# Performance work log

Measured on AMD Instinct MI355X. Metric: run time of the kernel, lower is better.

## Reference

```python
import jax, jax.numpy as jnp
import numpy as np

EMB, HID, NH = 512, 256, 8
DH = HID // NH
LN_EPS = 1e-5


def _mk(key, shape, scale=0.02):
    return jax.random.normal(key, shape, dtype=jnp.float32) * scale


def setup_inputs() -> dict:
    key = jax.random.key(0)
    ks = jax.random.split(key, 24)
    B, S = 8, 256
    return {
        "memory_embeddings": jax.random.normal(ks[0], (B, S, EMB), dtype=jnp.float32),
        # memory_encoder: Linear(512,256) -> LayerNorm -> ReLU -> Linear(256,256)
        "enc_w1": _mk(ks[1], (HID, EMB)), "enc_b1": jnp.zeros((HID,), jnp.float32),
        "ln_g": jnp.ones((HID,), jnp.float32), "ln_b": jnp.zeros((HID,), jnp.float32),
        "enc_w2": _mk(ks[2], (HID, HID)), "enc_b2": jnp.zeros((HID,), jnp.float32),
        # MultiheadAttention packed qkv + out proj
        "in_proj_w": _mk(ks[3], (3 * HID, HID)), "in_proj_b": jnp.zeros((3 * HID,), jnp.float32),
        "out_w": _mk(ks[4], (HID, HID)), "out_b": jnp.zeros((HID,), jnp.float32),
        # consistency head: Linear(256,128) -> ReLU -> Linear(128,1) -> Sigmoid
        "cons_w1": _mk(ks[5], (HID // 2, HID)), "cons_b1": jnp.zeros((HID // 2,), jnp.float32),
        "cons_w2": _mk(ks[6], (1, HID // 2)), "cons_b2": jnp.zeros((1,), jnp.float32),
        # hallucination detector
        "hall_w1": _mk(ks[7], (HID // 2, HID)), "hall_b1": jnp.zeros((HID // 2,), jnp.float32),
        "hall_w2": _mk(ks[8], (1, HID // 2)), "hall_b2": jnp.zeros((1,), jnp.float32),
        # contradiction analyzer: Linear(512,256) -> ReLU -> Linear(256,1) -> Sigmoid
        "con_w1": _mk(ks[9], (HID, 2 * HID)), "con_b1": jnp.zeros((HID,), jnp.float32),
        "con_w2": _mk(ks[10], (1, HID)), "con_b2": jnp.zeros((1,), jnp.float32),
    }


def _forward(memory_embeddings, enc_w1, enc_b1, ln_g, ln_b, enc_w2, enc_b2,
             in_proj_w, in_proj_b, out_w, out_b,
             cons_w1, cons_b1, cons_w2, cons_b2,
             hall_w1, hall_b1, hall_w2, hall_b2,
             con_w1, con_b1, con_w2, con_b2):
    B, S, _ = memory_embeddings.shape
    # --- memory encoder (dropout in eval mode = identity) ---
    h = memory_embeddings @ enc_w1.T + enc_b1                      # [B,S,HID]
    mu = h.mean(-1, keepdims=True)
    var = ((h - mu) ** 2).mean(-1, keepdims=True)
    h = (h - mu) * jax.lax.rsqrt(var + LN_EPS) * ln_g + ln_b
    mf = jax.nn.relu(h) @ enc_w2.T + enc_b2                        # [B,S,HID]
    # --- multihead self-attention (batch_first, averaged attn weights) ---
    qkv = mf @ in_proj_w.T + in_proj_b                              # [B,S,3H]
    q, k, v = jnp.split(qkv, 3, axis=-1)
    def heads(t):  # [B,S,H] -> [B,NH,S,DH]
        return t.reshape(B, S, NH, DH).transpose(0, 2, 1, 3)
    q, k, v = heads(q), heads(k), heads(v)
    scores = jnp.einsum('bhsd,bhtd->bhst', q, k) / jnp.sqrt(jnp.float32(DH))
    attn = jax.nn.softmax(scores, axis=-1)                          # [B,NH,S,S]
    ctx = jnp.einsum('bhst,bhtd->bhsd', attn, v)
    ctx = ctx.transpose(0, 2, 1, 3).reshape(B, S, HID)
    attended = ctx @ out_w.T + out_b                                # [B,S,HID]
    attn_weights = attn.mean(axis=1)                                # [B,S,S]
    # --- pooled heads ---
    pooled = attended.mean(axis=1)                                  # [B,HID]
    cons = jax.nn.sigmoid(jax.nn.relu(pooled @ cons_w1.T + cons_b1) @ cons_w2.T + cons_b2)[:, 0]
    hall = jax.nn.sigmoid(jax.nn.relu(pooled @ hall_w1.T + hall_b1) @ hall_w2.T + hall_b2)[:, 0]
    # --- contradiction matrix over all i<j pairs (vectorized gather/MLP/scatter) ---
    iu, ju = np.triu_indices(S, k=1)                                # static indices
    Wa, Wb = con_w1[:, :HID], con_w1[:, HID:]                       # split concat-linear
    a = mf @ Wa.T                                                   # [B,S,HID]
    b = mf @ Wb.T
    hid = jax.nn.relu(a[:, iu] + b[:, ju] + con_b1)                 # [B,P,HID]
    sc = jax.nn.sigmoid(hid @ con_w2.T + con_b2)[..., 0]            # [B,P]
    M = jnp.zeros((B, S, S), dtype=mf.dtype)
    M = M.at[:, iu, ju].set(sc)
    M = M.at[:, ju, iu].set(sc)
    return cons, hall, M, attn_weights


def reference(memory_embeddings, enc_w1, enc_b1, ln_g, ln_b, enc_w2, enc_b2,
              in_proj_w, in_proj_b, out_w, out_b,
              cons_w1, cons_b1, cons_w2, cons_b2,
              hall_w1, hall_b1, hall_w2, hall_b2,
              con_w1, con_b1, con_w2, con_b2):
    return _forward(memory_embeddings, enc_w1, enc_b1, ln_g, ln_b, enc_w2, enc_b2,
                    in_proj_w, in_proj_b, out_w, out_b,
                    cons_w1, cons_b1, cons_w2, cons_b2,
                    hall_w1, hall_b1, hall_w2, hall_b2,
                    con_w1, con_b1, con_w2, con_b2)
```

## Files before the change

### kernel.cpp

```cpp
#include <hip/hip_runtime.h>
#include <math.h>

typedef __attribute__((ext_vector_type(8))) short bf16x8;
typedef __attribute__((ext_vector_type(4))) float f32x4;

__device__ __forceinline__ short f2b(float f) {
  union { float f; unsigned u; } v; v.f = f;
  unsigned u = v.u + 0x7fffu + ((v.u >> 16) & 1u);
  return (short)(u >> 16);
}

__device__ __forceinline__ bf16x8 cvt8(float4 a, float4 b) {
  bf16x8 r;
  r[0] = f2b(a.x); r[1] = f2b(a.y); r[2] = f2b(a.z); r[3] = f2b(a.w);
  r[4] = f2b(b.x); r[5] = f2b(b.y); r[6] = f2b(b.z); r[7] = f2b(b.w);
  return r;
}

__global__ __launch_bounds__(512) void k_enc(
    const float* __restrict__ me,
    const float* __restrict__ w1f, const float* __restrict__ b1,
    const float* __restrict__ g, const float* __restrict__ lb,
    const float* __restrict__ w2f, const float* __restrict__ b2,
    unsigned short* __restrict__ mfb, float* __restrict__ poolctx) {
  __shared__ float hh[16 * 260];
  __shared__ unsigned short rA[16 * 264];
  __shared__ unsigned short mfs[16 * 256];
  int tid = threadIdx.x, lane = tid & 63, w = tid >> 6;
  int row0 = blockIdx.x * 16;
  int m = lane & 15, q = lane >> 4;
  if (blockIdx.x == 0) {
    float4 z = {0.f, 0.f, 0.f, 0.f};
    ((float4*)poolctx)[tid] = z;
  }
  {
    f32x4 acc0 = (f32x4){0.f, 0.f, 0.f, 0.f};
    f32x4 acc1 = (f32x4){0.f, 0.f, 0.f, 0.f};
    const float* ap = me + (size_t)(row0 + m) * 512 + q * 8;
    const float* bp0 = w1f + (size_t)(w * 32 + m) * 512 + q * 8;
    const float* bp1 = w1f + (size_t)(w * 32 + 16 + m) * 512 + q * 8;
    float4 pa[4][2], pb[4][2][2];
#pragma unroll
    for (int d = 0; d < 4; ++d) {
      pa[d][0] = *(const float4*)(ap + d * 32);
      pa[d][1] = *(const float4*)(ap + d * 32 + 4);
      pb[d][0][0] = *(const float4*)(bp0 + d * 32);
      pb[d][0][1] = *(const float4*)(bp0 + d * 32 + 4);
      pb[d][1][0] = *(const float4*)(bp1 + d * 32);
      pb[d][1][1] = *(const float4*)(bp1 + d * 32 + 4);
    }
#pragma unroll
    for (int it = 0; it < 16; ++it) {
      int slot = it & 3;
      float4 a0 = pa[slot][0], a1 = pa[slot][1];
      float4 b00 = pb[slot][0][0], b01 = pb[slot][0][1];
      float4 b10 = pb[slot][1][0], b11 = pb[slot][1][1];
      if (it + 4 < 16) {
        pa[slot][0] = *(const float4*)(ap + (it + 4) * 32);
        pa[slot][1] = *(const float4*)(ap + (it + 4) * 32 + 4);
        pb[slot][0][0] = *(const float4*)(bp0 + (it + 4) * 32);
        pb[slot][0][1] = *(const float4*)(bp0 + (it + 4) * 32 + 4);
        pb[slot][1][0] = *(const float4*)(bp1 + (it + 4) * 32);
        pb[slot][1][1] = *(const float4*)(bp1 + (it + 4) * 32 + 4);
      }
      bf16x8 af = cvt8(a0, a1);
      acc0 = __builtin_amdgcn_mfma_f32_16x16x32_bf16(af, cvt8(b00, b01), acc0, 0, 0, 0);
      acc1 = __builtin_amdgcn_mfma_f32_16x16x32_bf16(af, cvt8(b10, b11), acc1, 0, 0, 0);
    }
#pragma unroll
    for (int nt = 0; nt < 2; ++nt) {
      int col = w * 32 + nt * 16 + m;
      float bias = b1[col];
      f32x4 a = nt ? acc1 : acc0;
#pragma unroll
      for (int reg = 0; reg < 4; ++reg)
        hh[(q * 4 + reg) * 260 + col] = a[reg] + bias;
    }
  }
  __syncthreads();
  {
    float4 g4 = *(const float4*)(g + lane * 4);
    float4 lb4 = *(const float4*)(lb + lane * 4);
#pragma unroll
    for (int rr = 0; rr < 2; ++rr) {
      int r = w * 2 + rr;
      float4 v = *(const float4*)&hh[r * 260 + lane * 4];
      float s1 = v.x + v.y + v.z + v.w;
      float s2 = v.x * v.x + v.y * v.y + v.z * v.z + v.w * v.w;
#pragma unroll
      for (int o = 32; o > 0; o >>= 1) {
        s1 += __shfl_xor(s1, o, 64);
        s2 += __shfl_xor(s2, o, 64);
      }
      float mu = s1 * (1.f / 256.f);
      float var = s2 * (1.f / 256.f) - mu * mu;
      float rs = rsqrtf(var + 1e-5f);
      unsigned short y0 = (unsigned short)f2b(fmaxf((v.x - mu) * rs * g4.x + lb4.x, 0.f));
      unsigned short y1 = (unsigned short)f2b(fmaxf((v.y - mu) * rs * g4.y + lb4.y, 0.f));
      unsigned short y2 = (unsigned short)f2b(fmaxf((v.z - mu) * rs * g4.z + lb4.z, 0.f));
      unsigned short y3 = (unsigned short)f2b(fmaxf((v.w - mu) * rs * g4.w + lb4.w, 0.f));
      uint2 pk;
      pk.x = (unsigned)y0 | ((unsigned)y1 << 16);
      pk.y = (unsigned)y2 | ((unsigned)y3 << 16);
      *(uint2*)&rA[r * 264 + lane * 4] = pk;
    }
  }
  __syncthreads();
  {
    f32x4 acc0 = (f32x4){0.f, 0.f, 0.f, 0.f};
    f32x4 acc1 = (f32x4){0.f, 0.f, 0.f, 0.f};
    const float* cp0 = w2f + (size_t)(w * 32 + m) * 256 + q * 8;
    const float* cp1 = w2f + (size_t)(w * 32 + 16 + m) * 256 + q * 8;
    float4 pb[4][2][2];
#pragma unroll
    for (int d = 0; d < 4; ++d) {
      pb[d][0][0] = *(const float4*)(cp0 + d * 32);
      pb[d][0][1] = *(const float4*)(cp0 + d * 32 + 4);
      pb[d][1][0] = *(const float4*)(cp1 + d * 32);
      pb[d][1][1] = *(const float4*)(cp1 + d * 32 + 4);
    }
#pragma unroll
    for (int it = 0; it < 8; ++it) {
      int slot = it & 3;
      float4 b00 = pb[slot][0][0], b01 = pb[slot][0][1];
      float4 b10 = pb[slot][1][0], b11 = pb[slot][1][1];
      if (it + 4 < 8) {
        pb[slot][0][0] = *(const float4*)(cp0 + (it + 4) * 32);
        pb[slot][0][1] = *(const float4*)(cp0 + (it + 4) * 32 + 4);
        pb[slot][1][0] = *(const float4*)(cp1 + (it + 4) * 32);
        pb[slot][1][1] = *(const float4*)(cp1 + (it + 4) * 32 + 4);
      }
      bf16x8 af = *(const bf16x8*)&rA[m * 264 + it * 32 + q * 8];
      acc0 = __builtin_amdgcn_mfma_f32_16x16x32_bf16(af, cvt8(b00, b01), acc0, 0, 0, 0);
      acc1 = __builtin_amdgcn_mfma_f32_16x16x32_bf16(af, cvt8(b10, b11), acc1, 0, 0, 0);
    }
#pragma unroll
    for (int nt = 0; nt < 2; ++nt) {
      int col = w * 32 + nt * 16 + m;
      float bias = b2[col];
      f32x4 a = nt ? acc1 : acc0;
#pragma unroll
      for (int reg = 0; reg < 4; ++reg)
        mfs[(q * 4 + reg) * 256 + col] = (unsigned short)f2b(a[reg] + bias);
    }
  }
  __syncthreads();
  {
    const uint4* src = (const uint4*)mfs;
    uint4* dst = (uint4*)(mfb + (size_t)row0 * 256);
    dst[tid] = src[tid];
  }
}

__global__ __launch_bounds__(256) void k_proj5(
    const unsigned short* __restrict__ mfb,
    const float* __restrict__ wq, const float* __restrict__ wc,
    const float* __restrict__ bq, const float* __restrict__ cb1,
    float* __restrict__ qkv, float* __restrict__ amat,
    float* __restrict__ bmat) {
  int tid = threadIdx.x, lane = tid & 63, w = tid >> 6;
  int row0 = blockIdx.x * 16;
  int part = blockIdx.y;
  int m = lane & 15, q = lane >> 4;
  const float* Wbase;
  size_t wstride;
  if (part < 3) { Wbase = wq + (size_t)part * 256 * 256; wstride = 256; }
  else { Wbase = wc + (part == 4 ? 256 : 0); wstride = 512; }
  bf16x8 a[8];
#pragma unroll
  for (int ks = 0; ks < 8; ++ks)
    a[ks] = *(const bf16x8*)(mfb + (size_t)(row0 + m) * 256 + ks * 32 + q * 8);
  f32x4 acc[4];
#pragma unroll
  for (int i = 0; i < 4; ++i) acc[i] = (f32x4){0.f, 0.f, 0.f, 0.f};
  const float* bp[4];
#pragma unroll
  for (int nt = 0; nt < 4; ++nt)
    bp[nt] = Wbase + (size_t)(w * 64 + nt * 16 + m) * wstride + q * 8;
  float4 pb[4][4][2];
#pragma unroll
  for (int d = 0; d < 4; ++d)
#pragma unroll
    for (int nt = 0; nt < 4; ++nt) {
      pb[d][nt][0] = *(const float4*)(bp[nt] + d * 32);
      pb[d][nt][1] = *(const float4*)(bp[nt] + d * 32 + 4);
    }
#pragma unroll
  for (int it = 0; it < 8; ++it) {
    int slot = it & 3;
    float4 b0l = pb[slot][0][0], b0h = pb[slot][0][1];
    float4 b1l = pb[slot][1][0], b1h = pb[slot][1][1];
    float4 b2l = pb[slot][2][0], b2h = pb[slot][2][1];
    float4 b3l = pb[slot][3][0], b3h = pb[slot][3][1];
    if (it + 4 < 8) {
#pragma unroll
      for (int nt = 0; nt < 4; ++nt) {
        pb[slot][nt][0] = *(const float4*)(bp[nt] + (it + 4) * 32);
        pb[slot][nt][1] = *(const float4*)(bp[nt] + (it + 4) * 32 + 4);
      }
    }
    acc[0] = __builtin_amdgcn_mfma_f32_16x16x32_bf16(a[it], cvt8(b0l, b0h), acc[0], 0, 0, 0);
    acc[1] = __builtin_amdgcn_mfma_f32_16x16x32_bf16(a[it], cvt8(b1l, b1h), acc[1], 0, 0, 0);
    acc[2] = __builtin_amdgcn_mfma_f32_16x16x32_bf16(a[it], cvt8(b2l, b2h), acc[2], 0, 0, 0);
    acc[3] = __builtin_amdgcn_mfma_f32_16x16x32_bf16(a[it], cvt8(b3l, b3h), acc[3], 0, 0, 0);
  }
#pragma unroll
  for (int nt = 0; nt < 4; ++nt) {
    int col = w * 64 + nt * 16 + m;
    float bias;
    float* dst;
    int ld;
    if (part < 3) { bias = bq[part * 256 + col]; dst = qkv + part * 256; ld = 768; }
    else if (part == 3) { bias = cb1[col]; dst = amat; ld = 256; }
    else { bias = 0.f; dst = bmat; ld = 256; }
#pragma unroll
    for (int reg = 0; reg < 4; ++reg) {
      int row = row0 + q * 4 + reg;
      dst[(size_t)row * ld + col] = acc[nt][reg] + bias;
    }
  }
}

__global__ __launch_bounds__(256) void k_attn_mfma(
    const float* __restrict__ qkv, unsigned short* __restrict__ attnb,
    float* __restrict__ poolctx) {
  __shared__ unsigned short qs[32 * 40];
  __shared__ unsigned short kb[256 * 40];
  __shared__ unsigned short vt[32 * 264];
  __shared__ unsigned short ps[32 * 264];
  __shared__ float redm[2][32];
  __shared__ float reds[2][32];
  int blk = blockIdx.x;
  int sg = blk & 7, bh = blk >> 3, h = bh & 7, b = bh >> 3;
  int tid = threadIdx.x, lane = tid & 63, w = tid >> 6;
  int m = lane & 15, q = lane >> 4;
  {
    int r = tid >> 3, c4 = tid & 7;
    float4 v = *(const float4*)(qkv + ((size_t)(b * 256 + sg * 32 + r)) * 768 + h * 32 + c4 * 4);
    unsigned short* dst = &qs[r * 40 + c4 * 4];
    dst[0] = (unsigned short)f2b(v.x); dst[1] = (unsigned short)f2b(v.y);
    dst[2] = (unsigned short)f2b(v.z); dst[3] = (unsigned short)f2b(v.w);
  }
#pragma unroll
  for (int i = 0; i < 8; ++i) {
    int f = i * 256 + tid;
    int r = f >> 3, c4 = f & 7;
    float4 v = *(const float4*)(qkv + ((size_t)(b * 256 + r)) * 768 + 256 + h * 32 + c4 * 4);
    unsigned short* dst = &kb[r * 40 + c4 * 4];
    dst[0] = (unsigned short)f2b(v.x); dst[1] = (unsigned short)f2b(v.y);
    dst[2] = (unsigned short)f2b(v.z); dst[3] = (unsigned short)f2b(v.w);
  }
  {
    const float4* vr = (const float4*)(qkv + ((size_t)(b * 256 + tid)) * 768 + 512 + h * 32);
#pragma unroll
    for (int d4 = 0; d4 < 8; ++d4) {
      float4 vv = vr[d4];
      vt[(d4 * 4 + 0) * 264 + tid] = (unsigned short)f2b(vv.x);
      vt[(d4 * 4 + 1) * 264 + tid] = (unsigned short)f2b(vv.y);
      vt[(d4 * 4 + 2) * 264 + tid] = (unsigned short)f2b(vv.z);
      vt[(d4 * 4 + 3) * 264 + tid] = (unsigned short)f2b(vv.w);
    }
  }
  __syncthreads();
  int mt = w & 1, ng = w >> 1;
  int lrow = mt * 16 + q * 4;
  f32x4 acc[8];
  {
    bf16x8 af = *(const bf16x8*)&qs[(mt * 16 + m) * 40 + q * 8];
#pragma unroll
    for (int nt = 0; nt < 8; ++nt) {
      bf16x8 bf = *(const bf16x8*)&kb[(ng * 128 + nt * 16 + m) * 40 + q * 8];
      acc[nt] = __builtin_amdgcn_mfma_f32_16x16x32_bf16(
          af, bf, (f32x4){0.f, 0.f, 0.f, 0.f}, 0, 0, 0);
    }
  }
  const float scale = 0.17677669529663689f;
#pragma unroll
  for (int nt = 0; nt < 8; ++nt)
#pragma unroll
    for (int reg = 0; reg < 4; ++reg) acc[nt][reg] *= scale;
  float pm[4];
#pragma unroll
  for (int reg = 0; reg < 4; ++reg) {
    float mx = acc[0][reg];
#pragma unroll
    for (int nt = 1; nt < 8; ++nt) mx = fmaxf(mx, acc[nt][reg]);
#pragma unroll
    for (int o = 1; o < 16; o <<= 1) mx = fmaxf(mx, __shfl_xor(mx, o, 64));
    pm[reg] = mx;
  }
  if (m == 0) {
#pragma unroll
    for (int reg = 0; reg < 4; ++reg) redm[ng][lrow + reg] = pm[reg];
  }
  __syncthreads();
  float inv[4];
  float psum[4];
#pragma unroll
  for (int reg = 0; reg < 4; ++reg) {
    float Mv = fmaxf(redm[0][lrow + reg], redm[1][lrow + reg]);
    float s = 0.f;
#pragma unroll
    for (int nt = 0; nt < 8; ++nt) {
      float e = __expf(acc[nt][reg] - Mv);
      acc[nt][reg] = e;
      s += e;
    }
#pragma unroll
    for (int o = 1; o < 16; o <<= 1) s += __shfl_xor(s, o, 64);
    psum[reg] = s;
  }
  if (m == 0) {
#pragma unroll
    for (int reg = 0; reg < 4; ++reg) reds[ng][lrow + reg] = psum[reg];
  }
  __syncthreads();
#pragma unroll
  for (int reg = 0; reg < 4; ++reg)
    inv[reg] = 1.f / (reds[0][lrow + reg] + reds[1][lrow + reg]);
#pragma unroll
  for (int nt = 0; nt < 8; ++nt) {
    int t = ng * 128 + nt * 16 + m;
#pragma unroll
    for (int reg = 0; reg < 4; ++reg)
      ps[(lrow + reg) * 264 + t] = (unsigned short)f2b(acc[nt][reg] * inv[reg]);
  }
  __syncthreads();
  {
    int r = tid >> 3, seg = tid & 7;
    const uint4* src = (const uint4*)&ps[r * 264 + seg * 32];
    uint4* dst = (uint4*)(attnb + ((size_t)(bh * 256 + sg * 32 + r)) * 256 + seg * 32);
    dst[0] = src[0]; dst[1] = src[1]; dst[2] = src[2]; dst[3] = src[3];
  }
  {
    int dt = w >> 1;
    f32x4 a = (f32x4){0.f, 0.f, 0.f, 0.f};
#pragma unroll
    for (int ks = 0; ks < 256; ks += 32) {
      bf16x8 af = *(const bf16x8*)&ps[(mt * 16 + m) * 264 + ks + q * 8];
      bf16x8 bf = *(const bf16x8*)&vt[(dt * 16 + m) * 264 + ks + q * 8];
      a = __builtin_amdgcn_mfma_f32_16x16x32_bf16(af, bf, a, 0, 0, 0);
    }
    float colsum = a[0] + a[1] + a[2] + a[3];
    colsum += __shfl_xor(colsum, 16, 64);
    colsum += __shfl_xor(colsum, 32, 64);
    if (lane < 16)
      atomicAdd(&poolctx[b * 256 + h * 32 + dt * 16 + m], colsum);
  }
}

__global__ __launch_bounds__(256) void k_tail(
    const float* __restrict__ amat, const float* __restrict__ bmat,
    const float* __restrict__ conw2, const float* __restrict__ conb2,
    float* __restrict__ M,
    const unsigned short* __restrict__ attnb, float* __restrict__ out_aw,
    const float* __restrict__ poolctx,
    const float* __restrict__ outw, const float* __restrict__ outb,
    const float* __restrict__ cw1, const float* __restrict__ cb1h,
    const float* __restrict__ cw2, const float* __restrict__ cb2,
    const float* __restrict__ hw1, const float* __restrict__ hb1,
    const float* __restrict__ hw2, const float* __restrict__ hb2,
    float* __restrict__ out) {
  __shared__ float smem[32 * 132 * 2 + 256];
  int bx = blockIdx.x, tid = threadIdx.x;
  if (bx < 288) {
    float* As = smem;
    float* Bs = smem + 32 * 132;
    float* w2s = smem + 32 * 132 * 2;
    int b = bx / 36, tix = bx % 36;
    int it = 0, rem = tix;
    while (rem >= 8 - it) { rem -= 8 - it; ++it; }
    int jt = it + rem;
    int tj = tid & 15, ti = tid >> 4;
    w2s[tid] = conw2[tid];
    float acc00 = 0, acc01 = 0, acc10 = 0, acc11 = 0;
    const float* Ab = amat + ((size_t)(b * 256 + it * 32)) * 256;
    const float* Bb = bmat + ((size_t)(b * 256 + jt * 32)) * 256;
    for (int ch = 0; ch < 2; ++ch) {
      __syncthreads();
#pragma unroll
      for (int k = 0; k < 4; ++k) {
        int f = tid + k * 256;
        int r = f >> 5, c4 = f & 31;
        float4 va = *(const float4*)(Ab + (size_t)r * 256 + ch * 128 + c4 * 4);
        float4 vb = *(const float4*)(Bb + (size_t)r * 256 + ch * 128 + c4 * 4);
        *(float4*)&As[r * 132 + c4 * 4] = va;
        *(float4*)&Bs[r * 132 + c4 * 4] = vb;
      }
      __syncthreads();
      const float* a0 = As + (2 * ti) * 132;
      const float* a1 = a0 + 132;
      const float* b0 = Bs + (2 * tj) * 132;
      const float* b1 = b0 + 132;
      const float* w2c = w2s + ch * 128;
      for (int d = 0; d < 128; d += 4) {
        float4 wv = *(const float4*)&w2c[d];
        float4 av0 = *(const float4*)&a0[d];
        float4 av1 = *(const float4*)&a1[d];
        float4 bv0 = *(const float4*)&b0[d];
        float4 bv1 = *(const float4*)&b1[d];
        acc00 += fmaxf(av0.x + bv0.x, 0.f) * wv.x + fmaxf(av0.y + bv0.y, 0.f) * wv.y
               + fmaxf(av0.z + bv0.z, 0.f) * wv.z + fmaxf(av0.w + bv0.w, 0.f) * wv.w;
        acc01 += fmaxf(av0.x + bv1.x, 0.f) * wv.x + fmaxf(av0.y + bv1.y, 0.f) * wv.y
               + fmaxf(av0.z + bv1.z, 0.f) * wv.z + fmaxf(av0.w + bv1.w, 0.f) * wv.w;
        acc10 += fmaxf(av1.x + bv0.x, 0.f) * wv.x + fmaxf(av1.y + bv0.y, 0.f) * wv.y
               + fmaxf(av1.z + bv0.z, 0.f) * wv.z + fmaxf(av1.w + bv0.w, 0.f) * wv.w;
        acc11 += fmaxf(av1.x + bv1.x, 0.f) * wv.x + fmaxf(av1.y + bv1.y, 0.f) * wv.y
               + fmaxf(av1.z + bv1.z, 0.f) * wv.z + fmaxf(av1.w + bv1.w, 0.f) * wv.w;
      }
    }
    float c2 = conb2[0];
    float s00 = 1.f / (1.f + expf(-(acc00 + c2)));
    float s01 = 1.f / (1.f + expf(-(acc01 + c2)));
    float s10 = 1.f / (1.f + expf(-(acc10 + c2)));
    float s11 = 1.f / (1.f + expf(-(acc11 + c2)));
    float* Mb = M + ((size_t)b << 16);
    int i0 = it * 32 + 2 * ti, i1 = i0 + 1;
    int j0 = jt * 32 + 2 * tj, j1 = j0 + 1;
    if (it != jt) {
      Mb[i0 * 256 + j0] = s00; Mb[j0 * 256 + i0] = s00;
      Mb[i0 * 256 + j1] = s01; Mb[j1 * 256 + i0] = s01;
      Mb[i1 * 256 + j0] = s10; Mb[j0 * 256 + i1] = s10;
      Mb[i1 * 256 + j1] = s11; Mb[j1 * 256 + i1] = s11;
    } else {
      if (j0 > i0) { Mb[i0 * 256 + j0] = s00; Mb[j0 * 256 + i0] = s00; }
      else if (j0 == i0) Mb[i0 * 256 + j0] = 0.f;
      if (j1 > i0) { Mb[i0 * 256 + j1] = s01; Mb[j1 * 256 + i0] = s01; }
      if (j0 > i1) { Mb[i1 * 256 + j0] = s10; Mb[j0 * 256 + i1] = s10; }
      if (j1 > i1) { Mb[i1 * 256 + j1] = s11; Mb[j1 * 256 + i1] = s11; }
      else if (j1 == i1) Mb[i1 * 256 + j1] = 0.f;
    }
  } else if (bx < 544) {
    int gid = (bx - 288) * 256 + tid;
    int b = gid >> 13, e8 = gid & 8191;
    size_t e = (size_t)e8 * 8;
    float s0 = 0, s1 = 0, s2 = 0, s3 = 0, s4 = 0, s5 = 0, s6 = 0, s7 = 0;
#pragma unroll
    for (int h = 0; h < 8; ++h) {
      uint4 v = *(const uint4*)(attnb + (((size_t)(b * 8 + h)) << 16) + e);
      s0 += __uint_as_float(v.x << 16); s1 += __uint_as_float(v.x & 0xffff0000u);
      s2 += __uint_as_float(v.y << 16); s3 += __uint_as_float(v.y & 0xffff0000u);
      s4 += __uint_as_float(v.z << 16); s5 += __uint_as_float(v.z & 0xffff0000u);
      s6 += __uint_as_float(v.w << 16); s7 += __uint_as_float(v.w & 0xffff0000u);
    }
    float* dst = out_aw + ((size_t)b << 16) + e;
    float4 r0 = {s0 * 0.125f, s1 * 0.125f, s2 * 0.125f, s3 * 0.125f};
    float4 r1 = {s4 * 0.125f, s5 * 0.125f, s6 * 0.125f, s7 * 0.125f};
    *(float4*)dst = r0;
    *(float4*)(dst + 4) = r1;
  } else {
    float* pc = smem;
    float* psh = smem + 256;
    float* red = smem + 512;
    int b = bx - 544, j = tid;
    pc[j] = poolctx[b * 256 + j] * (1.f / 256.f);
    __syncthreads();
    float s = outb[j];
    const float4* wr = (const float4*)(outw + (size_t)j * 256);
    for (int k4 = 0; k4 < 64; ++k4) {
      float4 wv = wr[k4];
      const float* p = pc + k4 * 4;
      s += p[0] * wv.x + p[1] * wv.y + p[2] * wv.z + p[3] * wv.w;
    }
    psh[j] = s;
    __syncthreads();
    int jj = j & 127;
    bool isH = j >= 128;
    const float* w1 = isH ? hw1 : cw1;
    const float* bb1 = isH ? hb1 : cb1h;
    const float* w2 = isH ? hw2 : cw2;
    float a = bb1[jj];
    const float4* w1r = (const float4*)(w1 + (size_t)jj * 256);
    for (int k4 = 0; k4 < 64; ++k4) {
      float4 wv = w1r[k4];
      const float* p = psh + k4 * 4;
      a += p[0] * wv.x + p[1] * wv.y + p[2] * wv.z + p[3] * wv.w;
    }
    float v = fmaxf(a, 0.f) * w2[jj];
#pragma unroll
    for (int o = 32; o > 0; o >>= 1) v += __shfl_xor(v, o, 64);
    if ((j & 63) == 0) red[j >> 6] = v;
    __syncthreads();
    if (j == 0) {
      float c = red[0] + red[1] + cb2[0];
      float h = red[2] + red[3] + hb2[0];
      out[b] = 1.f / (1.f + expf(-c));
      out[8 + b] = 1.f / (1.f + expf(-h));
    }
  }
}

extern "C" void kernel_launch(void* const* d_in, const int* in_sizes, int n_in,
                              void* d_out, int out_size, void* d_ws, size_t ws_size,
                              hipStream_t stream) {
  const float* me        = (const float*)d_in[0];
  const float* enc_w1    = (const float*)d_in[1];
  const float* enc_b1    = (const float*)d_in[2];
  const float* ln_g      = (const float*)d_in[3];
  const float* ln_b      = (const float*)d_in[4];
  const float* enc_w2    = (const float*)d_in[5];
  const float* enc_b2    = (const float*)d_in[6];
  const float* in_proj_w = (const float*)d_in[7];
  const float* in_proj_b = (const float*)d_in[8];
  const float* out_w     = (const float*)d_in[9];
  const float* out_b     = (const float*)d_in[10];
  const float* cons_w1   = (const float*)d_in[11];
  const float* cons_b1   = (const float*)d_in[12];
  const float* cons_w2   = (const float*)d_in[13];
  const float* cons_b2   = (const float*)d_in[14];
  const float* hall_w1   = (const float*)d_in[15];
  const float* hall_b1   = (const float*)d_in[16];
  const float* hall_w2   = (const float*)d_in[17];
  const float* hall_b2   = (const float*)d_in[18];
  const float* con_w1    = (const float*)d_in[19];
  const float* con_b1    = (const float*)d_in[20];
  const float* con_w2    = (const float*)d_in[21];
  const float* con_b2    = (const float*)d_in[22];

  float* ws = (float*)d_ws;
  float* qkv  = ws;
  unsigned short* attnb = (unsigned short*)(ws + 1572864);
  float* amat = ws + 3670016;
  float* bmat = ws + 4194304;
  unsigned short* mfb = (unsigned short*)(ws + 4718592);
  float* poolctx = ws + 4980736;

  float* out    = (float*)d_out;
  float* out_M  = out + 16;
  float* out_aw = out + 16 + 524288;

  k_enc<<<128, 512, 0, stream>>>(me, enc_w1, enc_b1, ln_g, ln_b,
                                 enc_w2, enc_b2, mfb, poolctx);
  k_proj5<<<dim3(128, 5), 256, 0, stream>>>(mfb, in_proj_w, con_w1,
                                            in_proj_b, con_b1,
                                            qkv, amat, bmat);
  k_attn_mfma<<<512, 256, 0, stream>>>(qkv, attnb, poolctx);
  k_tail<<<552, 256, 0, stream>>>(amat, bmat, con_w2, con_b2, out_M,
                                  attnb, out_aw, poolctx,
                                  out_w, out_b,
                                  cons_w1, cons_b1, cons_w2, cons_b2,
                                  hall_w1, hall_b1, hall_w2, hall_b2, out);
}
```

Measured before the change: 194.1 us.

## Pre-convert projection weights to bf16 and store QKV in head-major layout

```diff
diff --git a/kernel.cpp b/kernel.cpp
--- a/kernel.cpp
+++ b/kernel.cpp
@@ -22,11 +22,29 @@
     const float* __restrict__ w1f, const float* __restrict__ b1,
     const float* __restrict__ g, const float* __restrict__ lb,
     const float* __restrict__ w2f, const float* __restrict__ b2,
-    unsigned short* __restrict__ mfb, float* __restrict__ poolctx) {
+    const float* __restrict__ in_proj_w, const float* __restrict__ con_w1,
+    unsigned short* __restrict__ mfb, unsigned short* __restrict__ wbf,
+    float* __restrict__ poolctx) {
   __shared__ float hh[16 * 260];
   __shared__ unsigned short rA[16 * 264];
   __shared__ unsigned short mfs[16 * 256];
-  int tid = threadIdx.x, lane = tid & 63, w = tid >> 6;
+  int tid = threadIdx.x;
+  if (blockIdx.x >= 128) {
+    int base = ((blockIdx.x - 128) * 512 + tid) * 4;
+#pragma unroll
+    for (int u = 0; u < 4; ++u) {
+      int idx = base + u;
+      float v;
+      if (idx < 196608) v = in_proj_w[idx];
+      else {
+        int i = idx - 196608, n = i >> 8, k = i & 255;
+        v = (n < 256) ? con_w1[n * 512 + k] : con_w1[(n - 256) * 512 + 256 + k];
+      }
+      wbf[idx] = (unsigned short)f2b(v);
+    }
+    return;
+  }
+  int lane = tid & 63, w = tid >> 6;
   int row0 = blockIdx.x * 16;
   int m = lane & 15, q = lane >> 4;
   if (blockIdx.x == 0) {
@@ -154,18 +172,15 @@
 
 __global__ __launch_bounds__(256) void k_proj5(
     const unsigned short* __restrict__ mfb,
-    const float* __restrict__ wq, const float* __restrict__ wc,
+    const unsigned short* __restrict__ wbf,
     const float* __restrict__ bq, const float* __restrict__ cb1,
-    float* __restrict__ qkv, float* __restrict__ amat,
-    float* __restrict__ bmat) {
+    float* __restrict__ qh, float* __restrict__ kh, float* __restrict__ vh,
+    float* __restrict__ amat, float* __restrict__ bmat) {
   int tid = threadIdx.x, lane = tid & 63, w = tid >> 6;
   int row0 = blockIdx.x * 16;
   int part = blockIdx.y;
   int m = lane & 15, q = lane >> 4;
-  const float* Wbase;
-  size_t wstride;
-  if (part < 3) { Wbase = wq + (size_t)part * 256 * 256; wstride = 256; }
-  else { Wbase = wc + (part == 4 ? 256 : 0); wstride = 512; }
+  const unsigned short* W = wbf + (size_t)part * 65536;
   bf16x8 a[8];
 #pragma unroll
   for (int ks = 0; ks < 8; ++ks)
@@ -173,56 +188,55 @@
   f32x4 acc[4];
 #pragma unroll
   for (int i = 0; i < 4; ++i) acc[i] = (f32x4){0.f, 0.f, 0.f, 0.f};
-  const float* bp[4];
-#pragma unroll
-  for (int nt = 0; nt < 4; ++nt)
-    bp[nt] = Wbase + (size_t)(w * 64 + nt * 16 + m) * wstride + q * 8;
-  float4 pb[4][4][2];
+  bf16x8 pb[4][4];
 #pragma unroll
   for (int d = 0; d < 4; ++d)
 #pragma unroll
-    for (int nt = 0; nt < 4; ++nt) {
-      pb[d][nt][0] = *(const float4*)(bp[nt] + d * 32);
-      pb[d][nt][1] = *(const float4*)(bp[nt] + d * 32 + 4);
-    }
+    for (int nt = 0; nt < 4; ++nt)
+      pb[d][nt] = *(const bf16x8*)(W + (size_t)(w * 64 + nt * 16 + m) * 256 + d * 32 + q * 8);
 #pragma unroll
   for (int it = 0; it < 8; ++it) {
     int slot = it & 3;
-    float4 b0l = pb[slot][0][0], b0h = pb[slot][0][1];
-    float4 b1l = pb[slot][1][0], b1h = pb[slot][1][1];
-    float4 b2l = pb[slot][2][0], b2h = pb[slot][2][1];
-    float4 b3l = pb[slot][3][0], b3h = pb[slot][3][1];
+    bf16x8 bl0 = pb[slot][0], bl1 = pb[slot][1];
+    bf16x8 bl2 = pb[slot][2], bl3 = pb[slot][3];
     if (it + 4 < 8) {
 #pragma unroll
-      for (int nt = 0; nt < 4; ++nt) {
-        pb[slot][nt][0] = *(const float4*)(bp[nt] + (it + 4) * 32);
-        pb[slot][nt][1] = *(const float4*)(bp[nt] + (it + 4) * 32 + 4);
-      }
-    }
-    acc[0] = __builtin_amdgcn_mfma_f32_16x16x32_bf16(a[it], cvt8(b0l, b0h), acc[0], 0, 0, 0);
-    acc[1] = __builtin_amdgcn_mfma_f32_16x16x32_bf16(a[it], cvt8(b1l, b1h), acc[1], 0, 0, 0);
-    acc[2] = __builtin_amdgcn_mfma_f32_16x16x32_bf16(a[it], cvt8(b2l, b2h), acc[2], 0, 0, 0);
-    acc[3] = __builtin_amdgcn_mfma_f32_16x16x32_bf16(a[it], cvt8(b3l, b3h), acc[3], 0, 0, 0);
+      for (int nt = 0; nt < 4; ++nt)
+        pb[slot][nt] = *(const bf16x8*)(W + (size_t)(w * 64 + nt * 16 + m) * 256 + (it + 4) * 32 + q * 8);
+    }
+    acc[0] = __builtin_amdgcn_mfma_f32_16x16x32_bf16(a[it], bl0, acc[0], 0, 0, 0);
+    acc[1] = __builtin_amdgcn_mfma_f32_16x16x32_bf16(a[it], bl1, acc[1], 0, 0, 0);
+    acc[2] = __builtin_amdgcn_mfma_f32_16x16x32_bf16(a[it], bl2, acc[2], 0, 0, 0);
+    acc[3] = __builtin_amdgcn_mfma_f32_16x16x32_bf16(a[it], bl3, acc[3], 0, 0, 0);
   }
 #pragma unroll
   for (int nt = 0; nt < 4; ++nt) {
     int col = w * 64 + nt * 16 + m;
-    float bias;
-    float* dst;
-    int ld;
-    if (part < 3) { bias = bq[part * 256 + col]; dst = qkv + part * 256; ld = 768; }
-    else if (part == 3) { bias = cb1[col]; dst = amat; ld = 256; }
-    else { bias = 0.f; dst = bmat; ld = 256; }
-#pragma unroll
-    for (int reg = 0; reg < 4; ++reg) {
-      int row = row0 + q * 4 + reg;
-      dst[(size_t)row * ld + col] = acc[nt][reg] + bias;
+    if (part < 3) {
+      float bias = bq[part * 256 + col];
+      float* dst = (part == 0) ? qh : (part == 1) ? kh : vh;
+      int h = col >> 5, d = col & 31;
+#pragma unroll
+      for (int reg = 0; reg < 4; ++reg) {
+        int row = row0 + q * 4 + reg;
+        int b = row >> 8, s = row & 255;
+        dst[(((size_t)(b * 8 + h)) * 256 + s) * 32 + d] = acc[nt][reg] + bias;
+      }
+    } else {
+      float bias = (part == 3) ? cb1[col] : 0.f;
+      float* dst = (part == 3) ? amat : bmat;
+#pragma unroll
+      for (int reg = 0; reg < 4; ++reg) {
+        int row = row0 + q * 4 + reg;
+        dst[(size_t)row * 256 + col] = acc[nt][reg] + bias;
+      }
     }
   }
 }
 
 __global__ __launch_bounds__(256) void k_attn_mfma(
-    const float* __restrict__ qkv, unsigned short* __restrict__ attnb,
+    const float* __restrict__ qh, const float* __restrict__ kh,
+    const float* __restrict__ vh, unsigned short* __restrict__ attnb,
     float* __restrict__ poolctx) {
   __shared__ unsigned short qs[32 * 40];
   __shared__ unsigned short kb[256 * 40];
@@ -235,23 +249,27 @@
   int tid = threadIdx.x, lane = tid & 63, w = tid >> 6;
   int m = lane & 15, q = lane >> 4;
   {
+    const float* qbase = qh + (((size_t)bh) * 256 + sg * 32) * 32;
+    float4 v = ((const float4*)qbase)[tid];
     int r = tid >> 3, c4 = tid & 7;
-    float4 v = *(const float4*)(qkv + ((size_t)(b * 256 + sg * 32 + r)) * 768 + h * 32 + c4 * 4);
     unsigned short* dst = &qs[r * 40 + c4 * 4];
     dst[0] = (unsigned short)f2b(v.x); dst[1] = (unsigned short)f2b(v.y);
     dst[2] = (unsigned short)f2b(v.z); dst[3] = (unsigned short)f2b(v.w);
   }
-#pragma unroll
-  for (int i = 0; i < 8; ++i) {
-    int f = i * 256 + tid;
-    int r = f >> 3, c4 = f & 7;
-    float4 v = *(const float4*)(qkv + ((size_t)(b * 256 + r)) * 768 + 256 + h * 32 + c4 * 4);
-    unsigned short* dst = &kb[r * 40 + c4 * 4];
-    dst[0] = (unsigned short)f2b(v.x); dst[1] = (unsigned short)f2b(v.y);
-    dst[2] = (unsigned short)f2b(v.z); dst[3] = (unsigned short)f2b(v.w);
-  }
-  {
-    const float4* vr = (const float4*)(qkv + ((size_t)(b * 256 + tid)) * 768 + 512 + h * 32);
+  {
+    const float4* kbase = (const float4*)(kh + ((size_t)bh) * 256 * 32);
+#pragma unroll
+    for (int i = 0; i < 8; ++i) {
+      int f = i * 256 + tid;
+      float4 v = kbase[f];
+      int r = f >> 3, c4 = f & 7;
+      unsigned short* dst = &kb[r * 40 + c4 * 4];
+      dst[0] = (unsigned short)f2b(v.x); dst[1] = (unsigned short)f2b(v.y);
+      dst[2] = (unsigned short)f2b(v.z); dst[3] = (unsigned short)f2b(v.w);
+    }
+  }
+  {
+    const float4* vr = (const float4*)(vh + (((size_t)bh) * 256 + tid) * 32);
 #pragma unroll
     for (int d4 = 0; d4 < 8; ++d4) {
       float4 vv = vr[d4];
@@ -518,23 +536,26 @@
   const float* con_b2    = (const float*)d_in[22];
 
   float* ws = (float*)d_ws;
-  float* qkv  = ws;
+  float* qh   = ws;
+  float* kh   = ws + 524288;
+  float* vh   = ws + 1048576;
   unsigned short* attnb = (unsigned short*)(ws + 1572864);
   float* amat = ws + 3670016;
   float* bmat = ws + 4194304;
   unsigned short* mfb = (unsigned short*)(ws + 4718592);
-  float* poolctx = ws + 4980736;
+  unsigned short* wbf = (unsigned short*)(ws + 4980736);
+  float* poolctx = ws + 5144576;
 
   float* out    = (float*)d_out;
   float* out_M  = out + 16;
   float* out_aw = out + 16 + 524288;
 
-  k_enc<<<128, 512, 0, stream>>>(me, enc_w1, enc_b1, ln_g, ln_b,
-                                 enc_w2, enc_b2, mfb, poolctx);
-  k_proj5<<<dim3(128, 5), 256, 0, stream>>>(mfb, in_proj_w, con_w1,
-                                            in_proj_b, con_b1,
-                                            qkv, amat, bmat);
-  k_attn_mfma<<<512, 256, 0, stream>>>(qkv, attnb, poolctx);
+  k_enc<<<288, 512, 0, stream>>>(me, enc_w1, enc_b1, ln_g, ln_b,
+                                 enc_w2, enc_b2, in_proj_w, con_w1,
+                                 mfb, wbf, poolctx);
+  k_proj5<<<dim3(128, 5), 256, 0, stream>>>(mfb, wbf, in_proj_b, con_b1,
+                                            qh, kh, vh, amat, bmat);
+  k_attn_mfma<<<512, 256, 0, stream>>>(qh, kh, vh, attnb, poolctx);
   k_tail<<<552, 256, 0, stream>>>(amat, bmat, con_w2, con_b2, out_M,
                                   attnb, out_aw, poolctx,
                                   out_w, out_b,
```

Result: faster. 180.9 us (-6.8%).
